# Optimization experiments

Hardware: AMD Instinct MI355X
Metric: run time of the kernel (lower is better)

Reference implementation:

```python
import jax, jax.numpy as jnp
import numpy as np

B, T, C = 4, 2048, 1024
N_HEAD = 16
HEAD_DIM = C // N_HEAD


def setup_inputs() -> dict:
    key = jax.random.key(0)
    ks = jax.random.split(key, 5)
    bound = 1.0 / np.sqrt(C)
    x = jax.random.normal(ks[0], (B, T, C), dtype=jnp.float32)
    W_attn = jax.random.uniform(ks[1], (C, 3 * C), minval=-bound, maxval=bound, dtype=jnp.float32)
    b_attn = jax.random.uniform(ks[2], (3 * C,), minval=-bound, maxval=bound, dtype=jnp.float32)
    W_proj = jax.random.uniform(ks[3], (C, C), minval=-bound, maxval=bound, dtype=jnp.float32)
    b_proj = jax.random.uniform(ks[4], (C,), minval=-bound, maxval=bound, dtype=jnp.float32)
    return {"x": x, "W_attn": W_attn, "b_attn": b_attn, "W_proj": W_proj, "b_proj": b_proj}


def reference(x, W_attn, b_attn, W_proj, b_proj):
    Bx, Tx, Cx = x.shape
    qkv = x @ W_attn + b_attn                       # [B,T,3C]
    q, k, v = jnp.split(qkv, 3, axis=2)
    # [B,T,C] -> [B,H,T,D]
    q = q.reshape(Bx, Tx, N_HEAD, HEAD_DIM).transpose(0, 2, 1, 3)
    k = k.reshape(Bx, Tx, N_HEAD, HEAD_DIM).transpose(0, 2, 1, 3)
    v = v.reshape(Bx, Tx, N_HEAD, HEAD_DIM).transpose(0, 2, 1, 3)
    scale = 1.0 / np.sqrt(HEAD_DIM).astype(np.float32)
    att = jnp.einsum('bhqd,bhkd->bhqk', q, k) * scale   # [B,H,T,T]
    causal = jnp.tril(jnp.ones((Tx, Tx), dtype=bool))
    att = jnp.where(causal[None, None], att, -jnp.inf)
    att = jax.nn.softmax(att, axis=-1)
    y = jnp.einsum('bhqk,bhkd->bhqd', att, v)           # [B,H,T,D]
    y = y.transpose(0, 2, 1, 3).reshape(Bx, Tx, Cx)
    return y @ W_proj + b_proj
```

## Files before the change

kernel.cpp:

```cpp
#include <hip/hip_runtime.h>

#define Bsz 4
#define Tn 2048
#define Cn 1024
#define Hn 16
#define Dn 64
#define Mn (Bsz * Tn)
#define NQKV (3 * Cn)
#define BH (Bsz * Hn)

typedef short bf16x8_t __attribute__((ext_vector_type(8)));
typedef float f32x4 __attribute__((ext_vector_type(4)));

static __device__ __forceinline__ float exp2_fast(float x) {
    return __builtin_amdgcn_exp2f(x);
}

static __device__ __forceinline__ unsigned short f2bf(float f) {
    union { float f; unsigned int u; } v; v.f = f;
    unsigned int r = v.u + 0x7FFFu + ((v.u >> 16) & 1u);
    return (unsigned short)(r >> 16);
}

static __device__ __forceinline__ unsigned int fbits(float f) {
    union { float f; unsigned int u; } v; v.f = f; return v.u;
}

static __device__ __forceinline__ bf16x8_t ld_frag(const unsigned short* p) {
    bf16x8_t r;
    *reinterpret_cast<float4*>(&r) = *reinterpret_cast<const float4*>(p);
    return r;
}

#define ASYNC_COPY16(gp, lp)                                                         \
    __builtin_amdgcn_global_load_lds((__attribute__((address_space(1))) void*)(gp),  \
                                     (__attribute__((address_space(3))) void*)(lp),  \
                                     16, 0, 0)

#define MFMA_B16(a, b, c) __builtin_amdgcn_mfma_f32_16x16x32_bf16(a, b, c, 0, 0, 0)

__global__ void cast_f32_bf16(const float* __restrict__ src,
                              unsigned short* __restrict__ dst, int n4) {
    int i = blockIdx.x * blockDim.x + threadIdx.x;
    if (i < n4) {
        float4 v = reinterpret_cast<const float4*>(src)[i];
        ushort4 o;
        o.x = f2bf(v.x); o.y = f2bf(v.y); o.z = f2bf(v.z); o.w = f2bf(v.w);
        reinterpret_cast<ushort4*>(dst)[i] = o;
    }
}

__global__ void transpose_cast(const float* __restrict__ src,
                               unsigned short* __restrict__ dst, int R, int Cc) {
    __shared__ float tile[32][33];
    int c0 = blockIdx.x * 32, r0 = blockIdx.y * 32;
    int tx = threadIdx.x & 31, ty = threadIdx.x >> 5;
#pragma unroll
    for (int i = 0; i < 4; i++)
        tile[ty + i * 8][tx] = src[(long)(r0 + ty + i * 8) * Cc + c0 + tx];
    __syncthreads();
#pragma unroll
    for (int i = 0; i < 4; i++)
        dst[(long)(c0 + ty + i * 8) * R + r0 + tx] = f2bf(tile[tx][ty + i * 8]);
}

static __device__ __forceinline__ void stage_tile(const unsigned short* __restrict__ G,
                                                  int rowBase, int Kd, int kb,
                                                  unsigned short* lds, int tid) {
    int r = tid >> 3;
    int sg = (tid & 7) ^ (r & 7);
    const unsigned short* gp = G + (long)(rowBase + r) * Kd + kb + sg * 8;
    unsigned short* lb = lds + (tid >> 6) * 512;
#pragma unroll
    for (int l = 0; l < 4; ++l)
        ASYNC_COPY16(gp + (long)(l * 64) * Kd, lb + l * 4096);
}

static __device__ __forceinline__ bf16x8_t frag(const unsigned short* lds, int row, int cs) {
    return ld_frag(lds + row * 64 + ((cs ^ (row & 7)) << 3));
}

template <int MODE>
__global__ __launch_bounds__(512) void gemm256(const unsigned short* __restrict__ A,
                                               const unsigned short* __restrict__ Bt,
                                               const float* __restrict__ bias,
                                               float* __restrict__ outF,
                                               unsigned short* __restrict__ Qb,
                                               unsigned short* __restrict__ Kb,
                                               unsigned short* __restrict__ Vt,
                                               int M, int N, int Kd, int NBN) {
    __shared__ __align__(16) unsigned short smem[4 * 16384];
    int tid = threadIdx.x;
    int lane = tid & 63, w = tid >> 6;
    int wm = w >> 2, wn = w & 3;
    int quad = lane >> 4, l15 = lane & 15;

    int nwg = gridDim.x, f = blockIdx.x;
    int cpx = nwg >> 3;
    int t = (f & 7) * cpx + (f >> 3);
    int bm = t / NBN, bn = t - bm * NBN;
    int m0 = bm << 8, n0 = bn << 8;
    int NT = Kd >> 6;

    unsigned short* Ab0 = smem;
    unsigned short* Ab1 = smem + 16384;
    unsigned short* Bb0 = smem + 32768;
    unsigned short* Bb1 = smem + 49152;

    stage_tile(A, m0, Kd, 0, Ab0, tid);
    stage_tile(Bt, n0, Kd, 0, Bb0, tid);
    stage_tile(A, m0, Kd, 64, Ab1, tid);
    stage_tile(Bt, n0, Kd, 64, Bb1, tid);
    asm volatile("s_waitcnt vmcnt(8)" ::: "memory");
    asm volatile("s_barrier" ::: "memory");

    f32x4 acc[8][4] = {};
    int arow = wm * 128 + l15;
    int brow = wn * 64 + l15;

#pragma unroll 1
    for (int kt = 0; kt < NT; ++kt) {
        unsigned short* Al = (kt & 1) ? Ab1 : Ab0;
        unsigned short* Bl = (kt & 1) ? Bb1 : Bb0;
        bf16x8_t a0k0[4], a1k0[4], a0k1[4], a1k1[4], bk0[4], bk1[4];

#pragma unroll
        for (int i = 0; i < 4; ++i) a0k0[i] = frag(Al, arow + i * 16, quad);
#pragma unroll
        for (int i = 0; i < 4; ++i) a1k0[i] = frag(Al, arow + 64 + i * 16, quad);
#pragma unroll
        for (int n = 0; n < 4; ++n) bk0[n] = frag(Bl, brow + n * 16, quad);
        asm volatile("s_barrier" ::: "memory");
        asm volatile("s_waitcnt lgkmcnt(0)" ::: "memory");
        __builtin_amdgcn_s_setprio(1);
#pragma unroll
        for (int i = 0; i < 4; ++i)
#pragma unroll
            for (int n = 0; n < 4; ++n)
                acc[i][n] = MFMA_B16(a0k0[i], bk0[n], acc[i][n]);
        __builtin_amdgcn_s_setprio(0);
        asm volatile("s_barrier" ::: "memory");

#pragma unroll
        for (int i = 0; i < 4; ++i) a0k1[i] = frag(Al, arow + i * 16, 4 + quad);
#pragma unroll
        for (int i = 0; i < 4; ++i) a1k1[i] = frag(Al, arow + 64 + i * 16, 4 + quad);
#pragma unroll
        for (int n = 0; n < 4; ++n) bk1[n] = frag(Bl, brow + n * 16, 4 + quad);
        asm volatile("s_barrier" ::: "memory");
        asm volatile("s_waitcnt lgkmcnt(0)" ::: "memory");
        __builtin_amdgcn_s_setprio(1);
#pragma unroll
        for (int i = 0; i < 4; ++i)
#pragma unroll
            for (int n = 0; n < 4; ++n)
                acc[4 + i][n] = MFMA_B16(a1k0[i], bk0[n], acc[4 + i][n]);
        __builtin_amdgcn_s_setprio(0);
        asm volatile("s_barrier" ::: "memory");

        if (kt + 2 < NT) stage_tile(A, m0, Kd, (kt + 2) * 64, Al, tid);
        asm volatile("s_barrier" ::: "memory");
        __builtin_amdgcn_s_setprio(1);
#pragma unroll
        for (int i = 0; i < 4; ++i)
#pragma unroll
            for (int n = 0; n < 4; ++n)
                acc[i][n] = MFMA_B16(a0k1[i], bk1[n], acc[i][n]);
        __builtin_amdgcn_s_setprio(0);
        asm volatile("s_barrier" ::: "memory");

        if (kt + 2 < NT) stage_tile(Bt, n0, Kd, (kt + 2) * 64, Bl, tid);
        asm volatile("s_barrier" ::: "memory");
        __builtin_amdgcn_s_setprio(1);
#pragma unroll
        for (int i = 0; i < 4; ++i)
#pragma unroll
            for (int n = 0; n < 4; ++n)
                acc[4 + i][n] = MFMA_B16(a1k1[i], bk1[n], acc[4 + i][n]);
        __builtin_amdgcn_s_setprio(0);
        if (kt + 2 < NT)
            asm volatile("s_waitcnt vmcnt(8)" ::: "memory");
        else if (kt + 1 < NT)
            asm volatile("s_waitcnt vmcnt(0)" ::: "memory");
        asm volatile("s_barrier" ::: "memory");
    }

#pragma unroll
    for (int mi = 0; mi < 8; ++mi)
#pragma unroll
        for (int n = 0; n < 4; ++n) {
            int col = n0 + wn * 64 + n * 16 + l15;
            float bval = bias[col];
#pragma unroll
            for (int rr = 0; rr < 4; ++rr) {
                int row = m0 + wm * 128 + mi * 16 + quad * 4 + rr;
                float val = acc[mi][n][rr] + bval;
                if (MODE == 0) {
                    outF[(long)row * N + col] = val;
                } else {
                    int seg = col >> 10, within = col & 1023;
                    int h = within >> 6, d = within & 63;
                    int b = row >> 11, tt = row & 2047;
                    int bh = b * Hn + h;
                    if (seg == 0) {
                        Qb[((long)bh * Tn + tt) * Dn + d] = f2bf(val * 0.18033688f);
                    } else if (seg == 1) {
                        Kb[((long)bh * Tn + tt) * Dn + d] = f2bf(val);
                    } else {
                        Vt[((long)bh * Dn + d) * Tn + tt] = f2bf(val);
                    }
                }
            }
        }
}

__global__ __launch_bounds__(256) void attn_kernel(const unsigned short* __restrict__ Qb,
                                                   const unsigned short* __restrict__ Kb,
                                                   const unsigned short* __restrict__ Vt,
                                                   unsigned short* __restrict__ Yb) {
    __shared__ __align__(16) unsigned short Ks[64 * 72];
    __shared__ __align__(16) unsigned short Vs[64 * 72];
    __shared__ __align__(16) unsigned short Plds[4][2][16 * 72];
    int tid = threadIdx.x, w = tid >> 6, lane = tid & 63;
    int quad = lane >> 4, l15 = lane & 15;

    int flat = blockIdx.y * 8 + blockIdx.x;
    int xcd = flat & 7, slot = flat >> 3;
    int bh = xcd * 8 + (slot >> 3);
    int qx = slot & 7;
    int b = bh >> 4, h = bh & 15;

    const unsigned short* Qh = Qb + (long)bh * Tn * Dn;
    const unsigned short* Kh = Kb + (long)bh * Tn * Dn;
    const unsigned short* Vh = Vt + (long)bh * Dn * Tn;

    int sr = tid >> 3;
    int sc = (tid & 7) * 8;

#pragma unroll 1
    for (int s = 0; s < 2; s++) {
        int qi = s ? (15 - qx) : qx;
        int q0b = qi * 128;
        int nt = 2 * qi + 2;

        bf16x8_t qf[2][2];
#pragma unroll
        for (int h2 = 0; h2 < 2; h2++) {
            int qrow = q0b + h2 * 64 + w * 16 + l15;
            qf[h2][0] = ld_frag(&Qh[qrow * Dn + quad * 8]);
            qf[h2][1] = ld_frag(&Qh[qrow * Dn + 32 + quad * 8]);
        }

        float m_run[2] = {-1e30f, -1e30f}, l_run[2] = {0.f, 0.f};
        f32x4 Of[2][4] = {};

        float4 kr0 = *reinterpret_cast<const float4*>(&Kh[sr * Dn + sc]);
        float4 kr1 = *reinterpret_cast<const float4*>(&Kh[(32 + sr) * Dn + sc]);
        float4 vr0 = *reinterpret_cast<const float4*>(&Vh[sr * Tn + sc]);
        float4 vr1 = *reinterpret_cast<const float4*>(&Vh[(32 + sr) * Tn + sc]);

#pragma unroll 1
        for (int t = 0; t < nt; t++) {
            int kt0 = t * 64;
            __syncthreads();
            *reinterpret_cast<float4*>(&Ks[sr * 72 + sc]) = kr0;
            *reinterpret_cast<float4*>(&Ks[(32 + sr) * 72 + sc]) = kr1;
            *reinterpret_cast<float4*>(&Vs[sr * 72 + sc]) = vr0;
            *reinterpret_cast<float4*>(&Vs[(32 + sr) * 72 + sc]) = vr1;
            if (t + 1 < nt) {
                int kn = kt0 + 64;
                kr0 = *reinterpret_cast<const float4*>(&Kh[(kn + sr) * Dn + sc]);
                kr1 = *reinterpret_cast<const float4*>(&Kh[(kn + 32 + sr) * Dn + sc]);
                vr0 = *reinterpret_cast<const float4*>(&Vh[sr * Tn + kn + sc]);
                vr1 = *reinterpret_cast<const float4*>(&Vh[(32 + sr) * Tn + kn + sc]);
            }
            __syncthreads();

            bool act0 = (kt0 <= q0b);

            f32x4 st[2][4];
#pragma unroll
            for (int ti = 0; ti < 4; ti++) {
                bf16x8_t ka0 = ld_frag(&Ks[(ti * 16 + l15) * 72 + quad * 8]);
                bf16x8_t ka1 = ld_frag(&Ks[(ti * 16 + l15) * 72 + 32 + quad * 8]);
                if (act0) {
                    f32x4 z = {};
                    z = __builtin_amdgcn_mfma_f32_16x16x32_bf16(ka0, qf[0][0], z, 0, 0, 0);
                    st[0][ti] = __builtin_amdgcn_mfma_f32_16x16x32_bf16(ka1, qf[0][1], z, 0, 0, 0);
                }
                f32x4 z1 = {};
                z1 = __builtin_amdgcn_mfma_f32_16x16x32_bf16(ka0, qf[1][0], z1, 0, 0, 0);
                st[1][ti] = __builtin_amdgcn_mfma_f32_16x16x32_bf16(ka1, qf[1][1], z1, 0, 0, 0);
            }

            bf16x8_t pa[2][2];
#pragma unroll
            for (int h2 = 0; h2 < 2; h2++) {
                int qbase = q0b + h2 * 64;
                if (h2 == 0 && !act0) continue;
                if (kt0 == qbase) {
                    int q_glob = qbase + w * 16 + l15;
#pragma unroll
                    for (int ti = 0; ti < 4; ti++)
#pragma unroll
                        for (int rr = 0; rr < 4; rr++)
                            if (kt0 + ti * 16 + quad * 4 + rr > q_glob) st[h2][ti][rr] = -1e30f;
                }
                float lmax = st[h2][0][0];
#pragma unroll
                for (int ti = 0; ti < 4; ti++)
#pragma unroll
                    for (int rr = 0; rr < 4; rr++) lmax = fmaxf(lmax, st[h2][ti][rr]);
                lmax = fmaxf(lmax, __shfl_xor(lmax, 16));
                lmax = fmaxf(lmax, __shfl_xor(lmax, 32));
                float m_new = fmaxf(m_run[h2], lmax);
                float alpha = exp2_fast(m_run[h2] - m_new);
                float lsum = 0.f;
#pragma unroll
                for (int ti = 0; ti < 4; ti++)
#pragma unroll
                    for (int rr = 0; rr < 4; rr++) {
                        float e = exp2_fast(st[h2][ti][rr] - m_new);
                        st[h2][ti][rr] = e;
                        lsum += e;
                    }
                lsum += __shfl_xor(lsum, 16);
                lsum += __shfl_xor(lsum, 32);
                l_run[h2] = l_run[h2] * alpha + lsum;
                m_run[h2] = m_new;
#pragma unroll
                for (int rr = 0; rr < 4; rr++) {
                    float a_rr = __shfl(alpha, quad * 4 + rr);
#pragma unroll
                    for (int dt = 0; dt < 4; dt++) Of[h2][dt][rr] *= a_rr;
                }
                unsigned short* Pw = &Plds[w][h2][0];
#pragma unroll
                for (int ti = 0; ti < 4; ti++) {
                    unsigned u0 = fbits(st[h2][ti][0]) + 0x8000u;
                    unsigned u1 = fbits(st[h2][ti][1]) + 0x8000u;
                    unsigned u2 = fbits(st[h2][ti][2]) + 0x8000u;
                    unsigned u3 = fbits(st[h2][ti][3]) + 0x8000u;
                    uint2 pk;
                    pk.x = __builtin_amdgcn_perm(u1, u0, 0x07060302);
                    pk.y = __builtin_amdgcn_perm(u3, u2, 0x07060302);
                    *reinterpret_cast<uint2*>(&Pw[l15 * 72 + ti * 16 + quad * 4]) = pk;
                }
#pragma unroll
                for (int kc = 0; kc < 2; kc++)
                    pa[h2][kc] = ld_frag(&Pw[l15 * 72 + kc * 32 + quad * 8]);
            }

#pragma unroll
            for (int kc = 0; kc < 2; kc++)
#pragma unroll
                for (int dt = 0; dt < 4; dt++) {
                    bf16x8_t vb = ld_frag(&Vs[(dt * 16 + l15) * 72 + kc * 32 + quad * 8]);
                    if (act0)
                        Of[0][dt] = __builtin_amdgcn_mfma_f32_16x16x32_bf16(pa[0][kc], vb, Of[0][dt], 0, 0, 0);
                    Of[1][dt] = __builtin_amdgcn_mfma_f32_16x16x32_bf16(pa[1][kc], vb, Of[1][dt], 0, 0, 0);
                }
        }

#pragma unroll
        for (int h2 = 0; h2 < 2; h2++) {
            int qw = q0b + h2 * 64 + w * 16;
#pragma unroll
            for (int rr = 0; rr < 4; rr++) {
                float linv = 1.f / __shfl(l_run[h2], quad * 4 + rr);
                int t = qw + quad * 4 + rr;
                long rowbase = ((long)(b * Tn + t)) * Cn + h * Dn;
#pragma unroll
                for (int dt = 0; dt < 4; dt++)
                    Yb[rowbase + dt * 16 + l15] = f2bf(Of[h2][dt][rr] * linv);
            }
        }
    }
}

extern "C" void kernel_launch(void* const* d_in, const int* in_sizes, int n_in,
                              void* d_out, int out_size, void* d_ws, size_t ws_size,
                              hipStream_t stream) {
    const float* x      = (const float*)d_in[0];
    const float* W_attn = (const float*)d_in[1];
    const float* b_attn = (const float*)d_in[2];
    const float* W_proj = (const float*)d_in[3];
    const float* b_proj = (const float*)d_in[4];
    float* out = (float*)d_out;

    unsigned short* xb      = (unsigned short*)d_ws;
    unsigned short* Wqkv_t  = xb + (size_t)Mn * Cn;
    unsigned short* Wproj_t = Wqkv_t + (size_t)NQKV * Cn;
    unsigned short* Qb      = Wproj_t + (size_t)Cn * Cn;
    unsigned short* Kb      = Qb + (size_t)BH * Tn * Dn;
    unsigned short* Vt      = Kb + (size_t)BH * Tn * Dn;
    unsigned short* Yb      = Vt + (size_t)BH * Tn * Dn;

    cast_f32_bf16<<<(Mn * Cn / 4 + 255) / 256, 256, 0, stream>>>(x, xb, Mn * Cn / 4);
    transpose_cast<<<dim3(NQKV / 32, Cn / 32), 256, 0, stream>>>(W_attn, Wqkv_t, Cn, NQKV);
    transpose_cast<<<dim3(Cn / 32, Cn / 32), 256, 0, stream>>>(W_proj, Wproj_t, Cn, Cn);

    gemm256<1><<<dim3((NQKV / 256) * (Mn / 256)), 512, 0, stream>>>(
        xb, Wqkv_t, b_attn, nullptr, Qb, Kb, Vt, Mn, NQKV, Cn, NQKV / 256);

    attn_kernel<<<dim3(8, BH), 256, 0, stream>>>(Qb, Kb, Vt, Yb);

    gemm256<0><<<dim3((Cn / 256) * (Mn / 256)), 512, 0, stream>>>(
        Yb, Wproj_t, b_proj, out, nullptr, nullptr, nullptr, Mn, Cn, Cn, Cn / 256);
}
```

Measured before the change: 321.8 us.

## Restructure GEMM pipeline into half-tile stages and defer softmax rescaling

The GEMM main loop is rewritten to process two K-tiles per iteration in four quadrant phases, with each global-to-LDS stage split into half-tiles interleaved between phases. The aim is finer-grained overlap of loads with MFMA work and fewer live fragment registers. In the attention kernel, the online-softmax rescale is skipped when the new max exceeds the running max by at most 8 (in exp2 units) across the whole wavefront. This avoids the exp and the accumulator multiplies at the cost of a larger dynamic range in the bf16 probabilities. It also adds s_setprio around the MFMA blocks.

```diff
diff --git a/kernel.cpp b/kernel.cpp
--- a/kernel.cpp
+++ b/kernel.cpp
@@ -64,21 +64,58 @@
         dst[(long)(c0 + ty + i * 8) * R + r0 + tx] = f2bf(tile[tx][ty + i * 8]);
 }
 
-static __device__ __forceinline__ void stage_tile(const unsigned short* __restrict__ G,
+static __device__ __forceinline__ void stage_half(const unsigned short* __restrict__ G,
                                                   int rowBase, int Kd, int kb,
                                                   unsigned short* lds, int tid) {
     int r = tid >> 3;
     int sg = (tid & 7) ^ (r & 7);
     const unsigned short* gp = G + (long)(rowBase + r) * Kd + kb + sg * 8;
     unsigned short* lb = lds + (tid >> 6) * 512;
-#pragma unroll
-    for (int l = 0; l < 4; ++l)
-        ASYNC_COPY16(gp + (long)(l * 64) * Kd, lb + l * 4096);
+    ASYNC_COPY16(gp, lb);
+    ASYNC_COPY16(gp + (long)64 * Kd, lb + 4096);
 }
 
 static __device__ __forceinline__ bf16x8_t frag(const unsigned short* lds, int row, int cs) {
     return ld_frag(lds + row * 64 + ((cs ^ (row & 7)) << 3));
 }
+
+#define PH_PRE()                                           \
+    do {                                                   \
+        asm volatile("s_barrier" ::: "memory");            \
+        asm volatile("s_waitcnt lgkmcnt(0)" ::: "memory"); \
+        __builtin_amdgcn_sched_barrier(0);                 \
+        __builtin_amdgcn_s_setprio(1);                     \
+    } while (0)
+
+#define PH_POST()                                \
+    do {                                         \
+        __builtin_amdgcn_s_setprio(0);           \
+        asm volatile("s_barrier" ::: "memory");  \
+    } while (0)
+
+#define LD_A(buf, MI0)                                                          \
+    do {                                                                        \
+        _Pragma("unroll") for (int mi = 0; mi < 4; ++mi)                        \
+            _Pragma("unroll") for (int kk = 0; kk < 2; ++kk)                    \
+                a[(MI0) + mi][kk] = frag(buf, arow + ((MI0) + mi) * 16, kk * 4 + quad); \
+    } while (0)
+
+#define LD_B(buf, N0)                                                           \
+    do {                                                                        \
+        _Pragma("unroll") for (int nn = 0; nn < 2; ++nn)                        \
+            _Pragma("unroll") for (int kk = 0; kk < 2; ++kk)                    \
+                b[(N0) + nn][kk] = frag(buf, brow + ((N0) + nn) * 16, kk * 4 + quad); \
+    } while (0)
+
+#define QUAD_MM(M4, N2)                                                         \
+    do {                                                                        \
+        _Pragma("unroll") for (int kk = 0; kk < 2; ++kk)                        \
+            _Pragma("unroll") for (int mi = 0; mi < 4; ++mi)                    \
+                _Pragma("unroll") for (int nn = 0; nn < 2; ++nn)                \
+                    acc[(M4) + mi][(N2) + nn] =                                 \
+                        MFMA_B16(a[(M4) + mi][kk], b[(N2) + nn][kk],            \
+                                 acc[(M4) + mi][(N2) + nn]);                    \
+    } while (0)
 
 template <int MODE>
 __global__ __launch_bounds__(512) void gemm256(const unsigned short* __restrict__ A,
@@ -107,81 +144,55 @@
     unsigned short* Bb0 = smem + 32768;
     unsigned short* Bb1 = smem + 49152;
 
-    stage_tile(A, m0, Kd, 0, Ab0, tid);
-    stage_tile(Bt, n0, Kd, 0, Bb0, tid);
-    stage_tile(A, m0, Kd, 64, Ab1, tid);
-    stage_tile(Bt, n0, Kd, 64, Bb1, tid);
-    asm volatile("s_waitcnt vmcnt(8)" ::: "memory");
-    asm volatile("s_barrier" ::: "memory");
+    stage_half(A,  m0,       Kd, 0,  Ab0,        tid);
+    stage_half(A,  m0 + 128, Kd, 0,  Ab0 + 8192, tid);
+    stage_half(Bt, n0,       Kd, 0,  Bb0,        tid);
+    stage_half(Bt, n0 + 128, Kd, 0,  Bb0 + 8192, tid);
+    stage_half(Bt, n0,       Kd, 64, Bb1,        tid);
+    stage_half(Bt, n0 + 128, Kd, 64, Bb1 + 8192, tid);
+    asm volatile("s_waitcnt vmcnt(4)" ::: "memory");
+    __builtin_amdgcn_s_barrier();
 
     f32x4 acc[8][4] = {};
     int arow = wm * 128 + l15;
     int brow = wn * 64 + l15;
+    int NI = NT >> 1;
 
 #pragma unroll 1
-    for (int kt = 0; kt < NT; ++kt) {
-        unsigned short* Al = (kt & 1) ? Ab1 : Ab0;
-        unsigned short* Bl = (kt & 1) ? Bb1 : Bb0;
-        bf16x8_t a0k0[4], a1k0[4], a0k1[4], a1k1[4], bk0[4], bk1[4];
-
-#pragma unroll
-        for (int i = 0; i < 4; ++i) a0k0[i] = frag(Al, arow + i * 16, quad);
-#pragma unroll
-        for (int i = 0; i < 4; ++i) a1k0[i] = frag(Al, arow + 64 + i * 16, quad);
-#pragma unroll
-        for (int n = 0; n < 4; ++n) bk0[n] = frag(Bl, brow + n * 16, quad);
+    for (int it = 0; it < NI; ++it) {
+        int kt1 = 2 * it + 1, kt2 = 2 * it + 2, kt3 = 2 * it + 3;
+        bf16x8_t a[8][2], b[4][2];
+
+        LD_A(Ab0, 0); LD_B(Bb0, 0);
+        stage_half(A, m0, Kd, kt1 * 64, Ab1, tid);
+        PH_PRE(); QUAD_MM(0, 0); PH_POST();
+        LD_B(Bb0, 2);
+        stage_half(A, m0 + 128, Kd, kt1 * 64, Ab1 + 8192, tid);
+        PH_PRE(); QUAD_MM(0, 2); PH_POST();
+        LD_A(Ab0, 4);
+        if (kt2 < NT) stage_half(Bt, n0, Kd, kt2 * 64, Bb0, tid);
+        PH_PRE(); QUAD_MM(4, 0); PH_POST();
+        if (kt2 < NT) stage_half(Bt, n0 + 128, Kd, kt2 * 64, Bb0 + 8192, tid);
+        PH_PRE(); QUAD_MM(4, 2);
+        __builtin_amdgcn_s_setprio(0);
+        if (kt2 < NT) asm volatile("s_waitcnt vmcnt(4)" ::: "memory");
+        else          asm volatile("s_waitcnt vmcnt(0)" ::: "memory");
         asm volatile("s_barrier" ::: "memory");
-        asm volatile("s_waitcnt lgkmcnt(0)" ::: "memory");
-        __builtin_amdgcn_s_setprio(1);
-#pragma unroll
-        for (int i = 0; i < 4; ++i)
-#pragma unroll
-            for (int n = 0; n < 4; ++n)
-                acc[i][n] = MFMA_B16(a0k0[i], bk0[n], acc[i][n]);
+
+        LD_A(Ab1, 0); LD_B(Bb1, 0);
+        if (kt2 < NT) stage_half(A, m0, Kd, kt2 * 64, Ab0, tid);
+        PH_PRE(); QUAD_MM(0, 0); PH_POST();
+        LD_B(Bb1, 2);
+        if (kt2 < NT) stage_half(A, m0 + 128, Kd, kt2 * 64, Ab0 + 8192, tid);
+        PH_PRE(); QUAD_MM(0, 2); PH_POST();
+        LD_A(Ab1, 4);
+        if (kt3 < NT) stage_half(Bt, n0, Kd, kt3 * 64, Bb1, tid);
+        PH_PRE(); QUAD_MM(4, 0); PH_POST();
+        if (kt3 < NT) stage_half(Bt, n0 + 128, Kd, kt3 * 64, Bb1 + 8192, tid);
+        PH_PRE(); QUAD_MM(4, 2);
         __builtin_amdgcn_s_setprio(0);
-        asm volatile("s_barrier" ::: "memory");
-
-#pragma unroll
-        for (int i = 0; i < 4; ++i) a0k1[i] = frag(Al, arow + i * 16, 4 + quad);
-#pragma unroll
-        for (int i = 0; i < 4; ++i) a1k1[i] = frag(Al, arow + 64 + i * 16, 4 + quad);
-#pragma unroll
-        for (int n = 0; n < 4; ++n) bk1[n] = frag(Bl, brow + n * 16, 4 + quad);
-        asm volatile("s_barrier" ::: "memory");
-        asm volatile("s_waitcnt lgkmcnt(0)" ::: "memory");
-        __builtin_amdgcn_s_setprio(1);
-#pragma unroll
-        for (int i = 0; i < 4; ++i)
-#pragma unroll
-            for (int n = 0; n < 4; ++n)
-                acc[4 + i][n] = MFMA_B16(a1k0[i], bk0[n], acc[4 + i][n]);
-        __builtin_amdgcn_s_setprio(0);
-        asm volatile("s_barrier" ::: "memory");
-
-        if (kt + 2 < NT) stage_tile(A, m0, Kd, (kt + 2) * 64, Al, tid);
-        asm volatile("s_barrier" ::: "memory");
-        __builtin_amdgcn_s_setprio(1);
-#pragma unroll
-        for (int i = 0; i < 4; ++i)
-#pragma unroll
-            for (int n = 0; n < 4; ++n)
-                acc[i][n] = MFMA_B16(a0k1[i], bk1[n], acc[i][n]);
-        __builtin_amdgcn_s_setprio(0);
-        asm volatile("s_barrier" ::: "memory");
-
-        if (kt + 2 < NT) stage_tile(Bt, n0, Kd, (kt + 2) * 64, Bl, tid);
-        asm volatile("s_barrier" ::: "memory");
-        __builtin_amdgcn_s_setprio(1);
-#pragma unroll
-        for (int i = 0; i < 4; ++i)
-#pragma unroll
-            for (int n = 0; n < 4; ++n)
-                acc[4 + i][n] = MFMA_B16(a1k1[i], bk1[n], acc[4 + i][n]);
-        __builtin_amdgcn_s_setprio(0);
-        if (kt + 2 < NT)
-            asm volatile("s_waitcnt vmcnt(8)" ::: "memory");
-        else if (kt + 1 < NT)
-            asm volatile("s_waitcnt vmcnt(0)" ::: "memory");
+        if (kt3 < NT) asm volatile("s_waitcnt vmcnt(4)" ::: "memory");
+        else          asm volatile("s_waitcnt vmcnt(0)" ::: "memory");
         asm volatile("s_barrier" ::: "memory");
     }
 
@@ -200,8 +211,8 @@
                 } else {
                     int seg = col >> 10, within = col & 1023;
                     int h = within >> 6, d = within & 63;
-                    int b = row >> 11, tt = row & 2047;
-                    int bh = b * Hn + h;
+                    int b2 = row >> 11, tt = row & 2047;
+                    int bh = b2 * Hn + h;
                     if (seg == 0) {
                         Qb[((long)bh * Tn + tt) * Dn + d] = f2bf(val * 0.18033688f);
                     } else if (seg == 1) {
@@ -279,6 +290,7 @@
             bool act0 = (kt0 <= q0b);
 
             f32x4 st[2][4];
+            __builtin_amdgcn_s_setprio(1);
 #pragma unroll
             for (int ti = 0; ti < 4; ti++) {
                 bf16x8_t ka0 = ld_frag(&Ks[(ti * 16 + l15) * 72 + quad * 8]);
@@ -292,6 +304,7 @@
                 z1 = __builtin_amdgcn_mfma_f32_16x16x32_bf16(ka0, qf[1][0], z1, 0, 0, 0);
                 st[1][ti] = __builtin_amdgcn_mfma_f32_16x16x32_bf16(ka1, qf[1][1], z1, 0, 0, 0);
             }
+            __builtin_amdgcn_s_setprio(0);
 
             bf16x8_t pa[2][2];
 #pragma unroll
@@ -313,8 +326,9 @@
                     for (int rr = 0; rr < 4; rr++) lmax = fmaxf(lmax, st[h2][ti][rr]);
                 lmax = fmaxf(lmax, __shfl_xor(lmax, 16));
                 lmax = fmaxf(lmax, __shfl_xor(lmax, 32));
-                float m_new = fmaxf(m_run[h2], lmax);
-                float alpha = exp2_fast(m_run[h2] - m_new);
+
+                bool defer = __all(lmax - m_run[h2] <= 8.f);
+                float m_new = defer ? m_run[h2] : fmaxf(m_run[h2], lmax);
                 float lsum = 0.f;
 #pragma unroll
                 for (int ti = 0; ti < 4; ti++)
@@ -326,13 +340,18 @@
                     }
                 lsum += __shfl_xor(lsum, 16);
                 lsum += __shfl_xor(lsum, 32);
-                l_run[h2] = l_run[h2] * alpha + lsum;
-                m_run[h2] = m_new;
-#pragma unroll
-                for (int rr = 0; rr < 4; rr++) {
-                    float a_rr = __shfl(alpha, quad * 4 + rr);
-#pragma unroll
-                    for (int dt = 0; dt < 4; dt++) Of[h2][dt][rr] *= a_rr;
+                if (defer) {
+                    l_run[h2] += lsum;
+                } else {
+                    float alpha = exp2_fast(m_run[h2] - m_new);
+                    l_run[h2] = l_run[h2] * alpha + lsum;
+                    m_run[h2] = m_new;
+#pragma unroll
+                    for (int rr = 0; rr < 4; rr++) {
+                        float a_rr = __shfl(alpha, quad * 4 + rr);
+#pragma unroll
+                        for (int dt = 0; dt < 4; dt++) Of[h2][dt][rr] *= a_rr;
+                    }
                 }
                 unsigned short* Pw = &Plds[w][h2][0];
 #pragma unroll
@@ -351,6 +370,7 @@
                     pa[h2][kc] = ld_frag(&Pw[l15 * 72 + kc * 32 + quad * 8]);
             }
 
+            __builtin_amdgcn_s_setprio(1);
 #pragma unroll
             for (int kc = 0; kc < 2; kc++)
 #pragma unroll
@@ -360,6 +380,7 @@
                         Of[0][dt] = __builtin_amdgcn_mfma_f32_16x16x32_bf16(pa[0][kc], vb, Of[0][dt], 0, 0, 0);
                     Of[1][dt] = __builtin_amdgcn_mfma_f32_16x16x32_bf16(pa[1][kc], vb, Of[1][dt], 0, 0, 0);
                 }
+            __builtin_amdgcn_s_setprio(0);
         }
 
 #pragma unroll
```

Result: no change. 318.8 us (-0.9%).
